# Kernel tuning notes

Measured on AMD Instinct MI355X. Metric: run time of the kernel, lower is better.

Reference implementation:

```python
import jax, jax.numpy as jnp
import numpy as np

B, N, FEAT, HID, H = 4, 2048, 512, 512, 8
HD = HID // H  # head_dim = 64


def rotate_half(x):
    # pairs along last dim: (x1, x2) -> (-x2, x1), interleaved
    x = x.reshape(*x.shape[:-1], -1, 2)
    x1, x2 = x[..., 0], x[..., 1]
    return jnp.stack((-x2, x1), axis=-1).reshape(*x.shape[:-2], -1)


def apply_rope(freqs, t):
    # freqs: [2, B, 1, N, HD] broadcasting over heads; t: [B, H, N, HD]
    return t * freqs[0] + rotate_half(t) * freqs[1]


def setup_inputs() -> dict:
    key = jax.random.key(0)
    ks = jax.random.split(key, 12)
    s = 0.02
    return {
        "x0": jax.random.normal(ks[0], (B, N, FEAT), jnp.float32),
        "x1": jax.random.normal(ks[1], (B, N, FEAT), jnp.float32),
        "encoding0": jax.random.normal(ks[2], (2, B, 1, N, HD), jnp.float32),
        "encoding1": jax.random.normal(ks[3], (2, B, 1, N, HD), jnp.float32),
        "Wqkv": jax.random.normal(ks[4], (FEAT, 3 * HID), jnp.float32) * s,
        "bqkv": jnp.zeros((3 * HID,), jnp.float32),
        "Wproj": jax.random.normal(ks[5], (HID, HID), jnp.float32) * s,
        "bproj": jnp.zeros((HID,), jnp.float32),
        "W1": jax.random.normal(ks[6], (FEAT + HID, 2 * FEAT), jnp.float32) * s,
        "b1": jnp.zeros((2 * FEAT,), jnp.float32),
        "ln_g": jnp.ones((2 * FEAT,), jnp.float32),
        "ln_b": jnp.zeros((2 * FEAT,), jnp.float32),
        "W2": jax.random.normal(ks[7], (2 * FEAT, FEAT), jnp.float32) * s,
        "b2": jnp.zeros((FEAT,), jnp.float32),
    }


def _block(x, enc, Wqkv, bqkv, Wproj, bproj, W1, b1, ln_g, ln_b, W2, b2):
    b, n, _ = x.shape
    qkv = x @ Wqkv + bqkv                                   # [B,N,3*HID]
    qkv = qkv.reshape(b, n, H, HD, 3).transpose(0, 2, 1, 3, 4)  # [B,H,N,HD,3]
    q, k, v = qkv[..., 0], qkv[..., 1], qkv[..., 2]
    q = apply_rope(enc, q)
    k = apply_rope(enc, k)
    scale = q.shape[-1] ** (-0.5)
    attn = jax.nn.softmax(jnp.einsum('bhid,bhjd->bhij', q, k) * scale, axis=-1)
    o = jnp.einsum('bhij,bhjd->bhid', attn, v)              # [B,H,N,HD]
    message = o.transpose(0, 2, 1, 3).reshape(b, n, HID) @ Wproj + bproj
    h = jnp.concatenate([x, message], axis=-1) @ W1 + b1    # [B,N,2*FEAT]
    mu = h.mean(-1, keepdims=True)
    var = ((h - mu) ** 2).mean(-1, keepdims=True)
    h = (h - mu) * jax.lax.rsqrt(var + 1e-5) * ln_g + ln_b
    return x + jax.nn.gelu(h, approximate=False) @ W2 + b2


def reference(x0, x1, encoding0, encoding1, Wqkv, bqkv, Wproj, bproj, W1, b1, ln_g, ln_b, W2, b2):
    p = (Wqkv, bqkv, Wproj, bproj, W1, b1, ln_g, ln_b, W2, b2)
    return (_block(x0, encoding0, *p), _block(x1, encoding1, *p))
```

## Files before the change

### kernel.cpp

```cpp
#include <hip/hip_runtime.h>
#include <hip/hip_bf16.h>

typedef __attribute__((ext_vector_type(8))) short   short8v;
typedef __attribute__((ext_vector_type(4))) short   short4v;
typedef __attribute__((ext_vector_type(8))) __bf16  bf16x8;
typedef __attribute__((ext_vector_type(4))) __bf16  bf16x4;
typedef __attribute__((ext_vector_type(4))) float   f32x4;

constexpr int Nn = 2048;

#define GLOAD_LDS(src, dst) \
  __builtin_amdgcn_global_load_lds((__attribute__((address_space(1))) unsigned int*)(src), \
                                   (__attribute__((address_space(3))) unsigned int*)(dst), 16, 0, 0)

#if __has_builtin(__builtin_amdgcn_exp2f)
#define EXP2F(x) __builtin_amdgcn_exp2f(x)
#else
#define EXP2F(x) exp2f(x)
#endif

#if __has_builtin(__builtin_amdgcn_mfma_f32_16x16x16bf16_1k)
#define HAVE_MFMA16 1
#define MFMA16(a, b, c) __builtin_amdgcn_mfma_f32_16x16x16bf16_1k(a, b, c, 0, 0, 0)
#else
#define HAVE_MFMA16 0
#endif

__device__ __forceinline__ unsigned pack_bf16(float lo, float hi) {
  union { __bf16 h[2]; unsigned u; } t;
  t.h[0] = (__bf16)lo; t.h[1] = (__bf16)hi;
  return t.u;
}

template<int AMODE, int BMODE, int EPI>
__global__ __launch_bounds__(256)
void gemm_mfma(const __bf16* __restrict__ A, const __bf16* __restrict__ A2,
               const __bf16* __restrict__ BT, const __bf16* __restrict__ BT2,
               const float* __restrict__ bias,
               const float* __restrict__ resid0, const float* __restrict__ resid1,
               float* __restrict__ Cf, __bf16* __restrict__ Cb, __bf16* __restrict__ Vt,
               int lda, int ldb, int ldb2, int ldc, int K1, int K)
{
  __shared__ __align__(16) __bf16 As[3][4096];
  __shared__ __align__(16) __bf16 Bs[3][4096];
  const int tid = threadIdx.x;
  const int w = tid >> 6, l = tid & 63;
  const int wr = w >> 1, wc = w & 1;
  const int lr = l & 15, lg = l >> 4;
  const int row0 = blockIdx.x * 128, col0 = blockIdx.y * 128;

  f32x4 acc[4][4];
#pragma unroll
  for (int i = 0; i < 4; ++i)
#pragma unroll
    for (int j = 0; j < 4; ++j) acc[i][j] = (f32x4){0.f, 0.f, 0.f, 0.f};

  const int srow = l >> 2;
  const int skk  = (((l & 3) ^ ((l >> 3) & 3))) * 8;

  auto stage = [&](int k0, int b) {
#pragma unroll
    for (int s = w; s < 8; s += 4) {
      const int m = s * 16 + srow;
      const __bf16* src;
      if constexpr (AMODE == 0) {
        src = A + (size_t)(row0 + m) * lda + k0 + skk;
      } else {
        const int gk = k0 + skk;
        src = (gk < K1) ? A  + (size_t)(row0 + m) * lda + gk
                        : A2 + (size_t)(row0 + m) * lda + (gk - K1);
      }
      GLOAD_LDS(src, &As[b][s * 512]);
    }
#pragma unroll
    for (int s = w; s < 8; s += 4) {
      const int n = s * 16 + srow;
      const __bf16* src;
      if constexpr (BMODE == 0) {
        src = BT + (size_t)(col0 + n) * ldb + k0 + skk;
      } else {
        const int gk = k0 + skk;
        src = (gk < K1) ? BT  + (size_t)(col0 + n) * ldb + gk
                        : BT2 + (size_t)(col0 + n) * ldb2 + (gk - K1);
      }
      GLOAD_LDS(src, &Bs[b][s * 512]);
    }
  };

  const int nt = K >> 5;
  stage(0, 0);
  if (nt > 1) stage(32, 1);
  asm volatile("s_waitcnt vmcnt(4)" ::: "memory");
  __builtin_amdgcn_sched_barrier(0);

  const int rsl = (lr >> 1) & 3;

  for (int t = 0; t < nt; ++t) {
    const int p = t % 3;
    __builtin_amdgcn_s_barrier();
    __builtin_amdgcn_sched_barrier(0);
    if (t + 2 < nt) stage((t + 2) * 32, (t + 2) % 3);
    bf16x8 af[4], bfv[4];
#pragma unroll
    for (int mi = 0; mi < 4; ++mi)
      af[mi] = *(const bf16x8*)&As[p][(wr * 64 + mi * 16 + lr) * 32 + (lg ^ rsl) * 8];
#pragma unroll
    for (int ni = 0; ni < 4; ++ni)
      bfv[ni] = *(const bf16x8*)&Bs[p][(wc * 64 + ni * 16 + lr) * 32 + (lg ^ rsl) * 8];
    __builtin_amdgcn_s_setprio(1);
#pragma unroll
    for (int mi = 0; mi < 4; ++mi)
#pragma unroll
      for (int ni = 0; ni < 4; ++ni)
        acc[mi][ni] = __builtin_amdgcn_mfma_f32_16x16x32_bf16(af[mi], bfv[ni], acc[mi][ni], 0, 0, 0);
    __builtin_amdgcn_s_setprio(0);
    if (t + 1 < nt) {
      if (t + 2 < nt) asm volatile("s_waitcnt vmcnt(4)" ::: "memory");
      else            asm volatile("s_waitcnt vmcnt(0)" ::: "memory");
    }
    __builtin_amdgcn_sched_barrier(0);
  }

  if constexpr (EPI == 4) {
    if (col0 >= 1024) {
      const int b2 = row0 >> 11;
#pragma unroll
      for (int mi = 0; mi < 4; ++mi)
#pragma unroll
        for (int ni = 0; ni < 4; ++ni) {
          const int col = col0 + wc * 64 + ni * 16 + lr;
          const int sec = col - 1024, h = sec >> 6, d = sec & 63;
          const int n0 = (row0 + wr * 64 + mi * 16 + lg * 4) & 2047;
          union { __bf16 h4[4]; short4 s4; } u;
#pragma unroll
          for (int r = 0; r < 4; ++r) u.h4[r] = (__bf16)(acc[mi][ni][r] + bias[col]);
          *(short4*)&Vt[(size_t)(b2 * 8 + h) * 131072 + (size_t)d * 2048 + n0] = u.s4;
        }
    } else {
      constexpr float SCQ = 0.125f * 1.44269504089f;
      const float* e = (row0 < 8192) ? resid0 : resid1;
#pragma unroll
      for (int mi = 0; mi < 4; ++mi)
#pragma unroll
        for (int ni = 0; ni < 4; ++ni) {
          const int col = col0 + wc * 64 + ni * 16 + lr;
          const int d = col & 63;
          const float sgn = (col & 1) ? 1.f : -1.f;
          const float scq = (col < 512) ? SCQ : 1.f;
#pragma unroll
          for (int r = 0; r < 4; ++r) {
            const int row = row0 + wr * 64 + mi * 16 + lg * 4 + r;
            const long bn = row & 8191;
            const float f0 = e[bn * 64 + d];
            const float f1 = e[524288 + bn * 64 + d];
            const float vb = acc[mi][ni][r] + bias[col];
            const float pb = __shfl_xor(vb, 1, 64);
            Cb[(size_t)row * 1024 + col] = (__bf16)((vb * f0 + sgn * pb * f1) * scq);
          }
        }
    }
    return;
  }

#pragma unroll
  for (int mi = 0; mi < 4; ++mi)
#pragma unroll
    for (int ni = 0; ni < 4; ++ni) {
      const int col = col0 + wc * 64 + ni * 16 + lr;
#pragma unroll
      for (int r = 0; r < 4; ++r) {
        const int row = row0 + wr * 64 + mi * 16 + lg * 4 + r;
        const float v = acc[mi][ni][r];
        if constexpr (EPI == 1) {
          Cb[(size_t)row * ldc + col] = (__bf16)(v + bias[col]);
        } else if constexpr (EPI == 3) {
          Cb[(size_t)row * ldc + col] = (__bf16)v;
        } else {
          const float rv = (float)Vt[(size_t)row * ldc + col];
          Cf[(size_t)row * ldc + col] = v + bias[col] + rv;
        }
      }
    }
}

__global__ __launch_bounds__(256, 2)
void fa_k(const __bf16* __restrict__ QK, const __bf16* __restrict__ Vg,
          __bf16* __restrict__ Ob)
{
  constexpr float FIXM = 8.f;
  __shared__ __align__(16) __bf16 Ks[3][4096];
  __shared__ __align__(16) __bf16 Vs[3][4096];
  const int tid = threadIdx.x;
  const int w = tid >> 6, l = tid & 63;
  const int lr = l & 15, lg = l >> 4;
  const int bid = blockIdx.x;
  const int qi = (bid >> 3) & 7;
  const int bh = (bid & 7) * 8 + (bid >> 6);
  const int b2 = bh >> 3, h = bh & 7;
  const __bf16* Qp = QK + (size_t)b2 * 2048 * 1024 + h * 64;
  const __bf16* Kp = Qp + 512;
  const __bf16* Vp = Vg + (size_t)bh * 131072;
  const int q0 = qi * 256 + w * 64;

  bf16x8 qf[4][2];
#pragma unroll
  for (int nf = 0; nf < 4; ++nf)
#pragma unroll
    for (int kk = 0; kk < 2; ++kk)
      qf[nf][kk] = *(const bf16x8*)&Qp[(size_t)(q0 + nf * 16 + lr) * 1024 + kk * 32 + lg * 8];

  f32x4 oacc[4][4];
#pragma unroll
  for (int i = 0; i < 4; ++i)
#pragma unroll
    for (int j = 0; j < 4; ++j) oacc[i][j] = (f32x4){0.f, 0.f, 0.f, 0.f};
  float rs[4] = {0.f, 0.f, 0.f, 0.f};

#if !HAVE_MFMA16
  const int Sa = (lg & 1) * 32 + lr, Sb2x = Sa + 16;
  const bool hi = (lg >> 1) & 1;
#endif

  auto stage = [&](int kv0, int b) {
#pragma unroll
    for (int i = 0; i < 2; ++i) {
      const int s = w + 4 * i;
      const int g = s * 64 + l, r = g >> 3, c = g & 7;
      GLOAD_LDS(Kp + (size_t)(kv0 + r) * 1024 + ((c ^ (r & 7)) * 8), &Ks[b][s * 512]);
      GLOAD_LDS(Vp + (size_t)r * 2048 + kv0 + ((c ^ (r & 7)) * 8), &Vs[b][s * 512]);
    }
  };

  stage(0, 0);
  stage(64, 1);
  asm volatile("s_waitcnt vmcnt(4)" ::: "memory");
  __builtin_amdgcn_sched_barrier(0);

  for (int t = 0; t < 32; ++t) {
    const int p = t % 3;
    __builtin_amdgcn_s_barrier();
    __builtin_amdgcn_sched_barrier(0);
    if (t + 2 < 32) stage((t + 2) * 64, (t + 2) % 3);

    f32x4 sacc[4][4];
#pragma unroll
    for (int i = 0; i < 4; ++i)
#pragma unroll
      for (int j = 0; j < 4; ++j) sacc[i][j] = (f32x4){0.f, 0.f, 0.f, 0.f};
#pragma unroll
    for (int kk = 0; kk < 2; ++kk) {
      bf16x8 ka[4];
#pragma unroll
      for (int mf = 0; mf < 4; ++mf)
        ka[mf] = *(const bf16x8*)&Ks[p][(mf * 16 + lr) * 64 + (((kk * 4 + lg) ^ (lr & 7)) * 8)];
      __builtin_amdgcn_s_setprio(1);
#pragma unroll
      for (int mf = 0; mf < 4; ++mf)
#pragma unroll
        for (int nf = 0; nf < 4; ++nf)
          sacc[mf][nf] = __builtin_amdgcn_mfma_f32_16x16x32_bf16(ka[mf], qf[nf][kk], sacc[mf][nf], 0, 0, 0);
      __builtin_amdgcn_s_setprio(0);
    }

    unsigned pkk[4][4][2];
#pragma unroll
    for (int nf = 0; nf < 4; ++nf) {
#pragma unroll
      for (int mf = 0; mf < 4; ++mf) {
        const float p0 = EXP2F(sacc[mf][nf][0] - FIXM);
        const float p1 = EXP2F(sacc[mf][nf][1] - FIXM);
        const float p2 = EXP2F(sacc[mf][nf][2] - FIXM);
        const float p3 = EXP2F(sacc[mf][nf][3] - FIXM);
        rs[nf] += (p0 + p1) + (p2 + p3);
        pkk[mf][nf][0] = pack_bf16(p0, p1);
        pkk[mf][nf][1] = pack_bf16(p2, p3);
      }
    }

#if HAVE_MFMA16
#pragma unroll
    for (int ks = 0; ks < 4; ++ks) {
      bf16x4 va[4];
#pragma unroll
      for (int mo = 0; mo < 4; ++mo) {
        const int g = (ks * 2 + (lg >> 1)) ^ (lr & 7);
        va[mo] = *(const bf16x4*)&Vs[p][(mo * 16 + lr) * 64 + g * 8 + (lg & 1) * 4];
      }
      __builtin_amdgcn_s_setprio(1);
#pragma unroll
      for (int mo = 0; mo < 4; ++mo)
#pragma unroll
        for (int nf = 0; nf < 4; ++nf)
          oacc[mo][nf] = MFMA16(__builtin_bit_cast(short4v, va[mo]),
                                __builtin_bit_cast(short4v, pkk[ks][nf]),
                                oacc[mo][nf]);
      __builtin_amdgcn_s_setprio(0);
    }
#else
#pragma unroll
    for (int kf = 0; kf < 2; ++kf) {
      bf16x8 va[4];
#pragma unroll
      for (int mo = 0; mo < 4; ++mo) {
        const int g = ((kf * 4 + lg) ^ (lr & 7));
        va[mo] = *(const bf16x8*)&Vs[p][(mo * 16 + lr) * 64 + g * 8];
      }
      bf16x8 bfr[4];
#pragma unroll
      for (int nf = 0; nf < 4; ++nf) {
        const unsigned s0 = hi ? pkk[kf * 2 + 1][nf][0] : pkk[kf * 2][nf][0];
        const unsigned s1 = hi ? pkk[kf * 2 + 1][nf][1] : pkk[kf * 2][nf][1];
        union { unsigned u[4]; bf16x8 v; } ub;
        ub.u[0] = (unsigned)__shfl((int)s0, Sa, 64);
        ub.u[1] = (unsigned)__shfl((int)s1, Sa, 64);
        ub.u[2] = (unsigned)__shfl((int)s0, Sb2x, 64);
        ub.u[3] = (unsigned)__shfl((int)s1, Sb2x, 64);
        bfr[nf] = ub.v;
      }
      __builtin_amdgcn_s_setprio(1);
#pragma unroll
      for (int mo = 0; mo < 4; ++mo)
#pragma unroll
        for (int nf = 0; nf < 4; ++nf)
          oacc[mo][nf] = __builtin_amdgcn_mfma_f32_16x16x32_bf16(va[mo], bfr[nf], oacc[mo][nf], 0, 0, 0);
      __builtin_amdgcn_s_setprio(0);
    }
#endif
    if (t < 31) {
      if (t + 2 < 32) asm volatile("s_waitcnt vmcnt(4)" ::: "memory");
      else            asm volatile("s_waitcnt vmcnt(0)" ::: "memory");
    }
    __builtin_amdgcn_sched_barrier(0);
  }

#pragma unroll
  for (int nf = 0; nf < 4; ++nf) {
    float ls = rs[nf];
    ls += __shfl_xor(ls, 16, 64);
    ls += __shfl_xor(ls, 32, 64);
    const float inv = 1.f / ls;
    const long row = (long)b2 * 2048 + q0 + nf * 16 + lr;
#pragma unroll
    for (int mo = 0; mo < 4; ++mo) {
      union { __bf16 h4[4]; short4 s4; } u;
#pragma unroll
      for (int r = 0; r < 4; ++r) u.h4[r] = (__bf16)(oacc[mo][nf][r] * inv);
      *(short4*)&Ob[row * 512 + h * 64 + mo * 16 + lg * 4] = u.s4;
    }
  }
}

__global__ __launch_bounds__(256)
void conv_f32_bf16_k(const float* __restrict__ s, __bf16* __restrict__ d)
{
  const long i = ((long)blockIdx.x * 256 + threadIdx.x) * 4;
  const float4 v = *(const float4*)&s[i];
  union { __bf16 h[4]; short4 sv; } u;
  u.h[0] = (__bf16)v.x; u.h[1] = (__bf16)v.y; u.h[2] = (__bf16)v.z; u.h[3] = (__bf16)v.w;
  *(short4*)&d[i] = u.sv;
}

__global__ __launch_bounds__(256)
void conv2_k(const float* __restrict__ x0, const float* __restrict__ x1,
             __bf16* __restrict__ d)
{
  const int bid = blockIdx.x;
  const float* s = (bid < 4096) ? x0 : x1;
  __bf16* dd = d + ((bid < 4096) ? 0 : 4194304);
  const long i = ((long)(bid & 4095) * 256 + threadIdx.x) * 4;
  const float4 v = *(const float4*)&s[i];
  union { __bf16 h[4]; short4 sv; } u;
  u.h[0] = (__bf16)v.x; u.h[1] = (__bf16)v.y; u.h[2] = (__bf16)v.z; u.h[3] = (__bf16)v.w;
  *(short4*)&dd[i] = u.sv;
}

__global__ __launch_bounds__(256)
void prep_wt_k(const float* __restrict__ Wqkv, const float* __restrict__ W1,
               const float* __restrict__ W2,
               __bf16* __restrict__ WqkvT, __bf16* __restrict__ W1T,
               __bf16* __restrict__ W2T)
{
  const int bid = blockIdx.x;
  const float* W; __bf16* WT; int K, N, bx, by; bool perm = false;
  if (bid < 768)       { W = Wqkv; WT = WqkvT; K = 512;  N = 1536; bx = bid % 48;          by = bid / 48;          perm = true; }
  else if (bid < 1792) { W = W1;   WT = W1T;   K = 1024; N = 1024; bx = (bid - 768) % 32;  by = (bid - 768) / 32; }
  else                 { W = W2;   WT = W2T;   K = 1024; N = 512;  bx = (bid - 1792) % 16; by = (bid - 1792) / 16; }
  __shared__ float t[32][33];
  const int n0 = bx * 32, k0 = by * 32;
  const int tx = threadIdx.x & 31, ty = threadIdx.x >> 5;
  for (int i = ty; i < 32; i += 8)
    t[i][tx] = W[(size_t)(k0 + i) * N + n0 + tx];
  __syncthreads();
  for (int i = ty; i < 32; i += 8) {
    int drow = n0 + i;
    if (perm) {
      const int h = drow / 192, rem = drow % 192;
      drow = (rem % 3) * 512 + h * 64 + rem / 3;
    }
    WT[(size_t)drow * K + k0 + tx] = (__bf16)t[tx][i];
  }
}

__global__ void bperm_k(const float* __restrict__ b, float* __restrict__ bp)
{
  const int i = blockIdx.x * 256 + threadIdx.x;
  if (i < 1536) {
    const int h = i / 192, rem = i % 192;
    bp[(rem % 3) * 512 + h * 64 + rem / 3] = b[i];
  }
}

__global__ __launch_bounds__(256)
void bfuse_k(const float* __restrict__ b1, const float* __restrict__ bproj,
             const float* __restrict__ W1, float* __restrict__ b1f)
{
  const int n = blockIdx.x * 256 + threadIdx.x;
  float s = b1[n];
  for (int m = 0; m < 512; ++m)
    s += bproj[m] * W1[(size_t)(512 + m) * 1024 + n];
  b1f[n] = s;
}

__global__ __launch_bounds__(256)
void ln_gelu_k(__bf16* __restrict__ Hb, const float* __restrict__ g,
               const float* __restrict__ be)
{
  __bf16* row = Hb + (size_t)blockIdx.x * 1024;
  const int tid = threadIdx.x, w = tid >> 6, l = tid & 63;
  __shared__ float ps[4][2];
  union { __bf16 h[4]; short4 sv; } u;
  u.sv = *(const short4*)&row[tid * 4];
  float v[4];
  float s = 0.f, sq = 0.f;
#pragma unroll
  for (int i = 0; i < 4; ++i) {
    v[i] = (float)u.h[i];
    s += v[i]; sq += v[i] * v[i];
  }
#pragma unroll
  for (int d = 32; d > 0; d >>= 1) {
    s  += __shfl_xor(s, d, 64);
    sq += __shfl_xor(sq, d, 64);
  }
  if (l == 0) { ps[w][0] = s; ps[w][1] = sq; }
  __syncthreads();
  s  = ps[0][0] + ps[1][0] + ps[2][0] + ps[3][0];
  sq = ps[0][1] + ps[1][1] + ps[2][1] + ps[3][1];
  const float mu = s * (1.f / 1024.f);
  const float var = sq * (1.f / 1024.f) - mu * mu;
  const float rstd = rsqrtf(var + 1e-5f);
#pragma unroll
  for (int i = 0; i < 4; ++i) {
    const int c = tid * 4 + i;
    const float y = (v[i] - mu) * rstd * g[c] + be[c];
    u.h[i] = (__bf16)(0.5f * y * (1.f + erff(y * 0.70710678118f)));
  }
  *(short4*)&row[tid * 4] = u.sv;
}

extern "C" void kernel_launch(void* const* d_in, const int* in_sizes, int n_in,
                              void* d_out, int out_size, void* d_ws, size_t ws_size,
                              hipStream_t stream)
{
  const float* x0   = (const float*)d_in[0];
  const float* x1   = (const float*)d_in[1];
  const float* enc0 = (const float*)d_in[2];
  const float* enc1 = (const float*)d_in[3];
  const float* Wqkv  = (const float*)d_in[4];
  const float* bqkv  = (const float*)d_in[5];
  const float* Wproj = (const float*)d_in[6];
  const float* bproj = (const float*)d_in[7];
  const float* W1    = (const float*)d_in[8];
  const float* b1    = (const float*)d_in[9];
  const float* ln_g  = (const float*)d_in[10];
  const float* ln_b  = (const float*)d_in[11];
  const float* W2    = (const float*)d_in[12];
  const float* b2    = (const float*)d_in[13];

  __bf16* wsb = (__bf16*)d_ws;
  __bf16* xb      = wsb;
  __bf16* WqkvT   = wsb + 8388608;
  __bf16* Wproj_b = wsb + 9175040;
  __bf16* W1T     = wsb + 9437184;
  __bf16* W2T     = wsb + 10485760;
  float*  bqkvp   = (float*)(wsb + 11010048);
  __bf16* qkvb    = wsb + 11013120;
  __bf16* Vt      = wsb + 27790336;
  __bf16* Ob      = wsb + 36178944;
  __bf16* WfT     = wsb + 44567552;
  float*  b1f     = (float*)(wsb + 45091840);
  __bf16* hb      = qkvb;

  prep_wt_k<<<2304, 256, 0, stream>>>(Wqkv, W1, W2, WqkvT, W1T, W2T);
  bperm_k<<<6, 256, 0, stream>>>(bqkv, bqkvp);
  conv_f32_bf16_k<<<256, 256, 0, stream>>>(Wproj, Wproj_b);
  gemm_mfma<0, 0, 3><<<dim3(8, 4), 256, 0, stream>>>(
      W1T + 512, nullptr, Wproj_b, nullptr, nullptr, nullptr, nullptr,
      nullptr, WfT, nullptr, 1024, 512, 0, 512, 0, 512);
  bfuse_k<<<4, 256, 0, stream>>>(b1, bproj, W1, b1f);

  conv2_k<<<8192, 256, 0, stream>>>(x0, x1, xb);

  gemm_mfma<0, 0, 4><<<dim3(128, 12), 256, 0, stream>>>(
      xb, nullptr, WqkvT, nullptr, bqkvp, enc0, enc1, nullptr, qkvb, Vt,
      512, 512, 0, 1024, 0, 512);
  fa_k<<<512, 256, 0, stream>>>(qkvb, Vt, Ob);
  gemm_mfma<1, 1, 1><<<dim3(128, 8), 256, 0, stream>>>(
      xb, Ob, W1T, WfT, b1f, nullptr, nullptr, nullptr, hb, nullptr,
      512, 1024, 512, 1024, 512, 1024);
  ln_gelu_k<<<16384, 256, 0, stream>>>(hb, ln_g, ln_b);
  gemm_mfma<0, 0, 2><<<dim3(128, 4), 256, 0, stream>>>(
      hb, nullptr, W2T, nullptr, b2, nullptr, nullptr, (float*)d_out, nullptr, xb,
      1024, 1024, 0, 512, 0, 1024);
}
```

Baseline: 311.4 us.

## Software-pipeline flash attention: overlap next tile's QK^T with current softmax·V

Restructures the attention main loop so the QK^T MFMAs for tile t+1 are issued alongside the softmax and PV work for tile t, using two score accumulator sets (A/B) and an unroll by two. The LDS ring grows from three to four K/V buffers and the prefetch depth rises to three tiles so the extra in-flight tile stays valid. The aim is to hide exp/pack latency behind independent matrix work. The cost is more registers (a second 64-float score array) and double the LDS, which may hurt occupancy under launch_bounds(256,2).

```diff
diff --git a/kernel.cpp b/kernel.cpp
--- a/kernel.cpp
+++ b/kernel.cpp
@@ -188,8 +188,8 @@
           __bf16* __restrict__ Ob)
 {
   constexpr float FIXM = 8.f;
-  __shared__ __align__(16) __bf16 Ks[3][4096];
-  __shared__ __align__(16) __bf16 Vs[3][4096];
+  __shared__ __align__(16) __bf16 Ks[4][4096];
+  __shared__ __align__(16) __bf16 Vs[4][4096];
   const int tid = threadIdx.x;
   const int w = tid >> 6, l = tid & 63;
   const int lr = l & 15, lg = l >> 4;
@@ -221,7 +221,8 @@
   const bool hi = (lg >> 1) & 1;
 #endif
 
-  auto stage = [&](int kv0, int b) {
+  auto stage = [&](int t, int b) {
+    const int kv0 = t * 64;
 #pragma unroll
     for (int i = 0; i < 2; ++i) {
       const int s = w + 4 * i;
@@ -231,52 +232,44 @@
     }
   };
 
-  stage(0, 0);
-  stage(64, 1);
-  asm volatile("s_waitcnt vmcnt(4)" ::: "memory");
-  __builtin_amdgcn_sched_barrier(0);
-
-  for (int t = 0; t < 32; ++t) {
-    const int p = t % 3;
-    __builtin_amdgcn_s_barrier();
-    __builtin_amdgcn_sched_barrier(0);
-    if (t + 2 < 32) stage((t + 2) * 64, (t + 2) % 3);
-
-    f32x4 sacc[4][4];
+  auto qkt = [&](int tt, f32x4 (&sc)[4][4]) {
+    const int pb = tt & 3;
 #pragma unroll
     for (int i = 0; i < 4; ++i)
 #pragma unroll
-      for (int j = 0; j < 4; ++j) sacc[i][j] = (f32x4){0.f, 0.f, 0.f, 0.f};
+      for (int j = 0; j < 4; ++j) sc[i][j] = (f32x4){0.f, 0.f, 0.f, 0.f};
 #pragma unroll
     for (int kk = 0; kk < 2; ++kk) {
       bf16x8 ka[4];
 #pragma unroll
       for (int mf = 0; mf < 4; ++mf)
-        ka[mf] = *(const bf16x8*)&Ks[p][(mf * 16 + lr) * 64 + (((kk * 4 + lg) ^ (lr & 7)) * 8)];
+        ka[mf] = *(const bf16x8*)&Ks[pb][(mf * 16 + lr) * 64 + (((kk * 4 + lg) ^ (lr & 7)) * 8)];
       __builtin_amdgcn_s_setprio(1);
 #pragma unroll
       for (int mf = 0; mf < 4; ++mf)
 #pragma unroll
         for (int nf = 0; nf < 4; ++nf)
-          sacc[mf][nf] = __builtin_amdgcn_mfma_f32_16x16x32_bf16(ka[mf], qf[nf][kk], sacc[mf][nf], 0, 0, 0);
+          sc[mf][nf] = __builtin_amdgcn_mfma_f32_16x16x32_bf16(ka[mf], qf[nf][kk], sc[mf][nf], 0, 0, 0);
       __builtin_amdgcn_s_setprio(0);
     }
-
+  };
+
+  auto smpv = [&](int tt, f32x4 (&sc)[4][4]) {
+    const int pb = tt & 3;
     unsigned pkk[4][4][2];
 #pragma unroll
     for (int nf = 0; nf < 4; ++nf) {
 #pragma unroll
       for (int mf = 0; mf < 4; ++mf) {
-        const float p0 = EXP2F(sacc[mf][nf][0] - FIXM);
-        const float p1 = EXP2F(sacc[mf][nf][1] - FIXM);
-        const float p2 = EXP2F(sacc[mf][nf][2] - FIXM);
-        const float p3 = EXP2F(sacc[mf][nf][3] - FIXM);
+        const float p0 = EXP2F(sc[mf][nf][0] - FIXM);
+        const float p1 = EXP2F(sc[mf][nf][1] - FIXM);
+        const float p2 = EXP2F(sc[mf][nf][2] - FIXM);
+        const float p3 = EXP2F(sc[mf][nf][3] - FIXM);
         rs[nf] += (p0 + p1) + (p2 + p3);
         pkk[mf][nf][0] = pack_bf16(p0, p1);
         pkk[mf][nf][1] = pack_bf16(p2, p3);
       }
     }
-
 #if HAVE_MFMA16
 #pragma unroll
     for (int ks = 0; ks < 4; ++ks) {
@@ -284,7 +277,7 @@
 #pragma unroll
       for (int mo = 0; mo < 4; ++mo) {
         const int g = (ks * 2 + (lg >> 1)) ^ (lr & 7);
-        va[mo] = *(const bf16x4*)&Vs[p][(mo * 16 + lr) * 64 + g * 8 + (lg & 1) * 4];
+        va[mo] = *(const bf16x4*)&Vs[pb][(mo * 16 + lr) * 64 + g * 8 + (lg & 1) * 4];
       }
       __builtin_amdgcn_s_setprio(1);
 #pragma unroll
@@ -303,7 +296,7 @@
 #pragma unroll
       for (int mo = 0; mo < 4; ++mo) {
         const int g = ((kf * 4 + lg) ^ (lr & 7));
-        va[mo] = *(const bf16x8*)&Vs[p][(mo * 16 + lr) * 64 + g * 8];
+        va[mo] = *(const bf16x8*)&Vs[pb][(mo * 16 + lr) * 64 + g * 8];
       }
       bf16x8 bfr[4];
 #pragma unroll
@@ -326,10 +319,33 @@
       __builtin_amdgcn_s_setprio(0);
     }
 #endif
-    if (t < 31) {
-      if (t + 2 < 32) asm volatile("s_waitcnt vmcnt(4)" ::: "memory");
-      else            asm volatile("s_waitcnt vmcnt(0)" ::: "memory");
-    }
+  };
+
+  f32x4 saccA[4][4], saccB[4][4];
+
+  stage(0, 0); stage(1, 1); stage(2, 2);
+  asm volatile("s_waitcnt vmcnt(4)" ::: "memory");
+  __builtin_amdgcn_sched_barrier(0);
+  __builtin_amdgcn_s_barrier();
+  __builtin_amdgcn_sched_barrier(0);
+  qkt(0, saccA);
+
+  for (int t2 = 0; t2 < 32; t2 += 2) {
+    __builtin_amdgcn_s_barrier();
+    __builtin_amdgcn_sched_barrier(0);
+    if (t2 + 3 < 32) stage(t2 + 3, (t2 + 3) & 3);
+    qkt(t2 + 1, saccB);
+    smpv(t2, saccA);
+    if (t2 + 3 < 32) asm volatile("s_waitcnt vmcnt(4)" ::: "memory");
+    else             asm volatile("s_waitcnt vmcnt(0)" ::: "memory");
+    __builtin_amdgcn_sched_barrier(0);
+    __builtin_amdgcn_s_barrier();
+    __builtin_amdgcn_sched_barrier(0);
+    if (t2 + 4 < 32) stage(t2 + 4, (t2 + 4) & 3);
+    if (t2 + 2 < 32) qkt(t2 + 2, saccA);
+    smpv(t2 + 1, saccB);
+    if (t2 + 4 < 32) asm volatile("s_waitcnt vmcnt(4)" ::: "memory");
+    else             asm volatile("s_waitcnt vmcnt(0)" ::: "memory");
     __builtin_amdgcn_sched_barrier(0);
   }
 
```

After: 615.8 us. 97.7% more time.
